# Performance work log

Measured on AMD Instinct MI355X. Metric: run time of the kernel, lower is better.

The kernel has to match this reference:

```python
import jax, jax.numpy as jnp
import numpy as np

N_LAYER = 4
N_HEAD = 8
D_HEAD = 64
D_MODEL = 512
D_INNER = 2048
NMT = 16  # num_mem_tokens
BSZ = 1
QLEN = 2048


def _rel_shift(x):
    # x: [i, j, b, n] -> Transformer-XL relative shift
    i, j, b, n = x.shape
    zero_pad = jnp.zeros((i, 1, b, n), dtype=x.dtype)
    x_padded = jnp.concatenate([zero_pad, x], axis=1)  # [i, j+1, b, n]
    x_padded = x_padded.reshape(j + 1, i, b, n)
    return x_padded[1:].reshape(i, j, b, n)


def _layer_norm(x, g, b):
    mu = jnp.mean(x, axis=-1, keepdims=True)
    var = jnp.mean(jnp.square(x - mu), axis=-1, keepdims=True)
    return (x - mu) / jnp.sqrt(var + 1e-5) * g + b


def setup_inputs() -> dict:
    key = jax.random.key(0)
    ks = jax.random.split(key, 12)
    s = 0.02
    return {
        "word_emb": jax.random.normal(ks[0], (BSZ, QLEN, D_MODEL), jnp.float32),
        "mem_tokens": jax.random.normal(ks[1], (NMT, BSZ, D_MODEL), jnp.float32),
        "Wqkv": jax.random.normal(ks[2], (N_LAYER, D_MODEL, 3 * N_HEAD * D_HEAD), jnp.float32) * s,
        "Wr": jax.random.normal(ks[3], (N_LAYER, D_MODEL, N_HEAD * D_HEAD), jnp.float32) * s,
        "Wo": jax.random.normal(ks[4], (N_LAYER, N_HEAD * D_HEAD, D_MODEL), jnp.float32) * s,
        "ln1_scale": jnp.ones((N_LAYER, D_MODEL), jnp.float32),
        "ln1_bias": jnp.zeros((N_LAYER, D_MODEL), jnp.float32),
        "ffn_W1": jax.random.normal(ks[5], (N_LAYER, D_MODEL, D_INNER), jnp.float32) * s,
        "ffn_b1": jnp.zeros((N_LAYER, D_INNER), jnp.float32),
        "ffn_W2": jax.random.normal(ks[6], (N_LAYER, D_INNER, D_MODEL), jnp.float32) * s,
        "ffn_b2": jnp.zeros((N_LAYER, D_MODEL), jnp.float32),
        "ln2_scale": jnp.ones((N_LAYER, D_MODEL), jnp.float32),
        "ln2_bias": jnp.zeros((N_LAYER, D_MODEL), jnp.float32),
        "r_w_bias": jax.random.normal(ks[7], (N_HEAD, D_HEAD), jnp.float32) * s,
        "r_r_bias": jax.random.normal(ks[8], (N_HEAD, D_HEAD), jnp.float32) * s,
    }


def reference(word_emb, mem_tokens, Wqkv, Wr, Wo, ln1_scale, ln1_bias,
              ffn_W1, ffn_b1, ffn_W2, ffn_b2, ln2_scale, ln2_bias,
              r_w_bias, r_r_bias):
    # word_emb: [B, Q, D] -> [Q, B, D]; prepend + append mem tokens (mem_at_end)
    w = jnp.transpose(word_emb, (1, 0, 2))
    w = jnp.concatenate([mem_tokens, w, mem_tokens], axis=0)  # [T, B, D]
    T, B = w.shape[0], w.shape[1]

    # causal mask (mlen=0) with mem-token exceptions, True = masked
    mask = jnp.triu(jnp.ones((T, T), dtype=bool), k=1)
    mask = mask.at[:NMT, :NMT].set(False)          # read-mem block attends to itself
    mask = mask.at[-NMT:, -NMT:].set(False)        # write-mem block attends to itself

    # sinusoidal relative positional embedding, pos_seq = T-1 .. 0
    inv_freq = 1.0 / (10000.0 ** (jnp.arange(0, D_MODEL, 2, dtype=jnp.float32) / D_MODEL))
    pos_seq = jnp.arange(T - 1, -1, -1.0, dtype=jnp.float32)
    sinusoid = pos_seq[:, None] * inv_freq[None, :]
    pos_emb = jnp.concatenate([jnp.sin(sinusoid), jnp.cos(sinusoid)], axis=-1)  # [T, D]

    scale = 1.0 / np.sqrt(D_HEAD)
    for l in range(N_LAYER):
        heads = w @ Wqkv[l]                                        # [T, B, 3*H*Dh]
        q, k, v = jnp.split(heads, 3, axis=-1)
        q = q.reshape(T, B, N_HEAD, D_HEAD)
        k = k.reshape(T, B, N_HEAD, D_HEAD)
        v = v.reshape(T, B, N_HEAD, D_HEAD)
        r = (pos_emb @ Wr[l]).reshape(T, N_HEAD, D_HEAD)           # [T, H, Dh]

        AC = jnp.einsum('ibnd,jbnd->ijbn', q + r_w_bias, k)
        BD = _rel_shift(jnp.einsum('ibnd,jnd->ijbn', q + r_r_bias, r))
        score = (AC + BD) * scale                                  # [T, T, B, H]
        score = jnp.where(mask[:, :, None, None], -1e30, score)
        prob = jax.nn.softmax(score, axis=1)
        attn_vec = jnp.einsum('ijbn,jbnd->ibnd', prob, v).reshape(T, B, N_HEAD * D_HEAD)

        w = _layer_norm(w + attn_vec @ Wo[l], ln1_scale[l], ln1_bias[l])  # post-LN
        ff = jax.nn.relu(w @ ffn_W1[l] + ffn_b1[l]) @ ffn_W2[l] + ffn_b2[l]
        w = _layer_norm(w + ff, ln2_scale[l], ln2_bias[l])
    return w  # [T, B, D]
```

## Files before the change

### kernel.cpp

```cpp
#include <hip/hip_runtime.h>
#include <hip/hip_bf16.h>
#include <math.h>

#define TT 2080
#define DM 512
#define DI 2048
#define NH 8
#define DH 64
#define NMTOK 16
#define NLAYER 4
#define QKV_N 1536
#define ATT_SCALE 0.125f
#define SPLIT 8
#define WT_STRIDE 3407872
#define QRP_HEAD 2200640

typedef short bf16x8 __attribute__((ext_vector_type(8)));
typedef float f32x4 __attribute__((ext_vector_type(4)));
typedef unsigned short ushort_t;

__device__ __forceinline__ ushort_t f2bf(float f) {
  __hip_bfloat16 h = __float2bfloat16(f);
  return *reinterpret_cast<ushort_t*>(&h);
}
__device__ __forceinline__ float bfbits2f(unsigned int hi_bits) {
  return __uint_as_float(hi_bits);
}
__device__ __forceinline__ float bf2f(ushort_t u) {
  return bfbits2f(((unsigned int)u) << 16);
}
__device__ __forceinline__ void unpack8(uint4 v, float* f) {
  f[0] = bfbits2f(v.x << 16); f[1] = bfbits2f(v.x & 0xffff0000u);
  f[2] = bfbits2f(v.y << 16); f[3] = bfbits2f(v.y & 0xffff0000u);
  f[4] = bfbits2f(v.z << 16); f[5] = bfbits2f(v.z & 0xffff0000u);
  f[6] = bfbits2f(v.w << 16); f[7] = bfbits2f(v.w & 0xffff0000u);
}
__device__ __forceinline__ unsigned int pack2(ushort_t lo, ushort_t hi) {
  return (unsigned int)lo | ((unsigned int)hi << 16);
}
__device__ __forceinline__ void barrier_lds() {
  asm volatile("s_waitcnt lgkmcnt(0)" ::: "memory");
  __builtin_amdgcn_s_barrier();
}
__device__ __forceinline__ size_t qr_rowbase(int i) {
  int m = i & 3;
  int r = (m == 0) ? 0 : (m == 1) ? 3 : (m == 2) ? 5 : 6;
  return (size_t)i * (i + 33) / 2 + 6 * (i >> 2) + r;
}

__global__ __launch_bounds__(256) void k_prep(
    const float* __restrict__ Wqkv, const float* __restrict__ Wr,
    const float* __restrict__ Wo, const float* __restrict__ W1,
    const float* __restrict__ W2, ushort_t* __restrict__ dstAll,
    const float* __restrict__ we, const float* __restrict__ mem,
    float* __restrict__ w, ushort_t* __restrict__ wb,
    ushort_t* __restrict__ posb) {
  const int tid = threadIdx.x;
  if (blockIdx.x >= 13312) {
    int idx = (blockIdx.x - 13312) * 256 + tid;
    if (idx >= TT * DM) return;
    int t = idx >> 9, d = idx & 511;
    float v;
    if (t < NMTOK) v = mem[t * DM + d];
    else if (t < NMTOK + 2048) v = we[(t - NMTOK) * DM + d];
    else v = mem[(t - (NMTOK + 2048)) * DM + d];
    w[idx] = v;
    wb[idx] = f2bf(v);
    float p = (float)(TT - 1 - t);
    int i2 = d & 255;
    float freq = 1.0f / powf(10000.f, ((float)(2 * i2)) / 512.f);
    float ang = p * freq;
    posb[idx] = f2bf((d < 256) ? sinf(ang) : cosf(ang));
    return;
  }
  __shared__ float tl[32][33];
  const int l = blockIdx.x / 3328;
  int idx = blockIdx.x % 3328;
  const float* src;
  ushort_t* dst = dstAll + (size_t)l * WT_STRIDE;
  int K, N, local;
  if (idx < 768)       { src = Wqkv + (size_t)l * 512 * 1536; K = 512;  N = 1536; local = idx; }
  else if (idx < 1024) { src = Wr   + (size_t)l * 512 * 512;  dst += 786432;  K = 512;  N = 512;  local = idx - 768; }
  else if (idx < 1280) { src = Wo   + (size_t)l * 512 * 512;  dst += 1048576; K = 512;  N = 512;  local = idx - 1024; }
  else if (idx < 2304) { src = W1   + (size_t)l * 512 * 2048; dst += 1310720; K = 512;  N = 2048; local = idx - 1280; }
  else                 { src = W2   + (size_t)l * 2048 * 512; dst += 2359296; K = 2048; N = 512;  local = idx - 2304; }
  const int ntiles = N / 32;
  const int n0 = (local % ntiles) * 32, k0 = (local / ntiles) * 32;
#pragma unroll
  for (int p = 0; p < 4; ++p) {
    int row = (tid >> 5) + 8 * p, col = tid & 31;
    tl[row][col] = src[(size_t)(k0 + row) * N + n0 + col];
  }
  __syncthreads();
#pragma unroll
  for (int p = 0; p < 4; ++p) {
    int n = (tid >> 5) + 8 * p, k = tid & 31;
    dst[(size_t)(n0 + n) * K + k0 + k] = f2bf(tl[k][n]);
  }
}

__device__ __forceinline__ void gemm32x64_body(const ushort_t* __restrict__ A,
                                               const ushort_t* __restrict__ Bt,
                                               const float* __restrict__ bias,
                                               float* __restrict__ C,
                                               ushort_t* __restrict__ Cb,
                                               ushort_t* __restrict__ qrb,
                                               const float* __restrict__ rrb,
                                               int N, int K, int flags,
                                               int m0, int n0) {
  __shared__ short As[32][72];
  __shared__ short Bs[64][72];
  const int tid = threadIdx.x;
  const int lane = tid & 63, wv = tid >> 6;
  const int wm = (wv >> 1) * 16, wn = (wv & 1) * 32;
  const int lm = lane & 15, quad = lane >> 4;
  const int sr = tid >> 3, sc8 = (tid & 7) * 8;

  f32x4 acc[2];
  acc[0] = (f32x4)(0.f); acc[1] = (f32x4)(0.f);

  auto loadA = [&](int k0) -> uint4 {
    return *(const uint4*)&A[(size_t)(m0 + sr) * K + k0 + sc8];
  };
  auto loadB = [&](int row, int k0) -> uint4 {
    return *(const uint4*)&Bt[(size_t)(n0 + row) * K + k0 + sc8];
  };

  uint4 aC = loadA(0), b0C = loadB(sr, 0), b1C = loadB(sr + 32, 0);

  for (int k0 = 0; k0 < K; k0 += 64) {
    const int kn = (k0 + 64 < K) ? k0 + 64 : k0;
    uint4 aN = loadA(kn), b0N = loadB(sr, kn), b1N = loadB(sr + 32, kn);
    barrier_lds();
    *(uint4*)&As[sr][sc8] = aC;
    *(uint4*)&Bs[sr][sc8] = b0C;
    *(uint4*)&Bs[sr + 32][sc8] = b1C;
    barrier_lds();
#pragma unroll
    for (int kk = 0; kk < 64; kk += 32) {
      bf16x8 a = *(const bf16x8*)&As[wm + lm][kk + quad * 8];
      bf16x8 b0 = *(const bf16x8*)&Bs[wn + lm][kk + quad * 8];
      bf16x8 b1 = *(const bf16x8*)&Bs[wn + 16 + lm][kk + quad * 8];
      acc[0] = __builtin_amdgcn_mfma_f32_16x16x32_bf16(a, b0, acc[0], 0, 0, 0);
      acc[1] = __builtin_amdgcn_mfma_f32_16x16x32_bf16(a, b1, acc[1], 0, 0, 0);
    }
    aC = aN; b0C = b0N; b1C = b1N;
  }
#pragma unroll
  for (int nt = 0; nt < 2; ++nt) {
    int col = n0 + wn + nt * 16 + lm;
    float bv = (flags & 1) ? bias[col] : 0.f;
#pragma unroll
    for (int t = 0; t < 4; ++t) {
      int row = m0 + wm + quad * 4 + t;
      float v = acc[nt][t] + bv;
      if (flags & 2) v = fmaxf(v, 0.f);
      if (flags & 4) Cb[(size_t)row * N + col] = f2bf(v);
      else C[(size_t)row * N + col] = v;
      if ((flags & 8) && col < DM)
        qrb[(size_t)row * DM + col] = f2bf(v + rrb[col]);
    }
  }
}

__global__ __launch_bounds__(256) void k_gemm_mfma(const ushort_t* __restrict__ A,
                                                   const ushort_t* __restrict__ Bt,
                                                   const float* __restrict__ bias,
                                                   float* __restrict__ C,
                                                   ushort_t* __restrict__ Cb,
                                                   int N, int K, int flags) {
  gemm32x64_body(A, Bt, bias, C, Cb, nullptr, nullptr, N, K, flags,
                 blockIdx.y * 32, blockIdx.x * 64);
}

__global__ __launch_bounds__(256) void k_gemm_qkvwr(const ushort_t* __restrict__ wb,
                                                    const ushort_t* __restrict__ posb,
                                                    const ushort_t* __restrict__ qkvT,
                                                    const ushort_t* __restrict__ wrT,
                                                    ushort_t* __restrict__ qkvb,
                                                    ushort_t* __restrict__ rbg,
                                                    ushort_t* __restrict__ qrb,
                                                    const float* __restrict__ rrb) {
  const int bx = blockIdx.x;
  if (bx < 24)
    gemm32x64_body(wb, qkvT, nullptr, nullptr, qkvb, qrb, rrb, QKV_N, DM,
                   (bx < 8) ? (4 | 8) : 4, blockIdx.y * 32, bx * 64);
  else
    gemm32x64_body(posb, wrT, nullptr, nullptr, rbg, nullptr, nullptr, DM, DM, 4,
                   blockIdx.y * 32, (bx - 24) * 64);
}

__global__ __launch_bounds__(256) void k_qr(const ushort_t* __restrict__ qrb,
                                            const ushort_t* __restrict__ rbg,
                                            ushort_t* __restrict__ qrp) {
  const int h = blockIdx.z;
  const int m0 = blockIdx.y * 32, n0 = blockIdx.x * 64;
  if (!(n0 == 0 || n0 + 63 >= TT - 32 - m0)) return;
  __shared__ short As[32][72];
  __shared__ short Bs[64][72];
  const int tid = threadIdx.x;
  const int lane = tid & 63, wv = tid >> 6;
  const int wm = (wv >> 1) * 16, wn = (wv & 1) * 32;
  const int lm = lane & 15, quad = lane >> 4;
  const int sr = tid >> 3, sc8 = (tid & 7) * 8;
  const uint4 zero4 = make_uint4(0, 0, 0, 0);

  *(uint4*)&As[sr][sc8] = *(const uint4*)&qrb[(size_t)(m0 + sr) * DM + h * DH + sc8];
  int br0 = n0 + sr, br1 = n0 + sr + 32;
  *(uint4*)&Bs[sr][sc8] =
      (br0 < TT) ? *(const uint4*)&rbg[(size_t)br0 * DM + h * DH + sc8] : zero4;
  *(uint4*)&Bs[sr + 32][sc8] =
      (br1 < TT) ? *(const uint4*)&rbg[(size_t)br1 * DM + h * DH + sc8] : zero4;
  __syncthreads();

  f32x4 acc[2];
  acc[0] = (f32x4)(0.f); acc[1] = (f32x4)(0.f);
#pragma unroll
  for (int kk = 0; kk < 64; kk += 32) {
    bf16x8 a = *(const bf16x8*)&As[wm + lm][kk + quad * 8];
    bf16x8 b0 = *(const bf16x8*)&Bs[wn + lm][kk + quad * 8];
    bf16x8 b1 = *(const bf16x8*)&Bs[wn + 16 + lm][kk + quad * 8];
    acc[0] = __builtin_amdgcn_mfma_f32_16x16x32_bf16(a, b0, acc[0], 0, 0, 0);
    acc[1] = __builtin_amdgcn_mfma_f32_16x16x32_bf16(a, b1, acc[1], 0, 0, 0);
  }
  const size_t hb = (size_t)h * QRP_HEAD;
#pragma unroll
  for (int nt = 0; nt < 2; ++nt) {
    int col = n0 + wn + nt * 16 + lm;
    if (col >= TT) continue;
#pragma unroll
    for (int t = 0; t < 4; ++t) {
      int row = m0 + wm + quad * 4 + t;
      float v = acc[nt][t];
      int p = row + col - (TT - 1);
      size_t rb = hb + qr_rowbase(row);
      if (p >= 0) qrp[rb + p] = f2bf(v);
      if (col < 16) qrp[rb + row + 1 + col] = f2bf(v);
    }
  }
}

__global__ __launch_bounds__(256) void k_attn(const ushort_t* __restrict__ qkv,
                                              const ushort_t* __restrict__ qrp,
                                              const float* __restrict__ rwb,
                                              float* __restrict__ mlP,
                                              ushort_t* __restrict__ opP) {
  const int h = blockIdx.y;
  const int qt = 64 - blockIdx.x;
  const int c = blockIdx.z;
  if (c > qt) return;
  const int i0 = qt * 32;
  const int tid = threadIdx.x;
  const int lane = tid & 63, wv = tid >> 6;
  const int lm = lane & 15, quad = lane >> 4;

  __shared__ short qw[32][72];
  __shared__ short ks_[32][72];
  __shared__ short vsT[64][70];
  __shared__ short pb[32][40];
  __shared__ float st[32][33];
  __shared__ float m_s[32], l_s[32], alpha_s[32];

  const int krr = tid >> 3, kc8 = (tid & 7) * 8;
  const int vrr = tid >> 4, vc4 = tid & 15;
  const int ii = tid >> 3, g = tid & 7, jjb = g * 4;
  const int i = i0 + ii;
  const size_t hb = (size_t)h * QRP_HEAD;
  const size_t qrRow = hb + qr_rowbase(i);
  const size_t qrRowW = hb + qr_rowbase(i + 1) + i + 2;

  auto loadK = [&](int j0) -> uint4 {
    return *(const uint4*)&qkv[(size_t)(j0 + krr) * QKV_N + DM + h * DH + kc8];
  };

  {
    uint4 qv = *(const uint4*)&qkv[(size_t)(i0 + krr) * QKV_N + h * DH + kc8];
    float f[8]; unpack8(qv, f);
    float4 w0 = *(const float4*)&rwb[h * DH + kc8];
    float4 w1 = *(const float4*)&rwb[h * DH + kc8 + 4];
    uint4 ow;
    ow.x = pack2(f2bf(f[0] + w0.x), f2bf(f[1] + w0.y));
    ow.y = pack2(f2bf(f[2] + w0.z), f2bf(f[3] + w0.w));
    ow.z = pack2(f2bf(f[4] + w1.x), f2bf(f[5] + w1.y));
    ow.w = pack2(f2bf(f[6] + w1.z), f2bf(f[7] + w1.w));
    *(uint4*)&qw[krr][kc8] = ow;
  }
  if (tid < 32) { m_s[tid] = -INFINITY; l_s[tid] = 0.f; }

  f32x4 oA = (f32x4)(0.f);
  f32x4 oB = (f32x4)(0.f);

  uint4 kcur = loadK(c * 32);
  const ushort_t* vp0 = &qkv[(size_t)(c * 32 + 2 * vrr) * QKV_N + 2 * DM + h * DH + vc4 * 4];
  uint2 v0cur = *(const uint2*)vp0, v1cur = *(const uint2*)(vp0 + QKV_N);

  for (int jt = c; jt <= qt; jt += SPLIT) {
    const int j0 = jt * 32;
    uint2 qr2 = *(const uint2*)&qrp[qrRow + j0 + jjb];
    const int jn = (jt + SPLIT <= qt) ? jt + SPLIT : jt;
    uint4 knext = loadK(jn * 32);
    const ushort_t* vpn = &qkv[(size_t)(jn * 32 + 2 * vrr) * QKV_N + 2 * DM + h * DH + vc4 * 4];
    uint2 v0n = *(const uint2*)vpn, v1n = *(const uint2*)(vpn + QKV_N);

    barrier_lds();
    *(uint4*)&ks_[krr][kc8] = kcur;
    {
      ushort_t a0 = (ushort_t)(v0cur.x & 0xffffu), a1 = (ushort_t)(v0cur.x >> 16);
      ushort_t a2 = (ushort_t)(v0cur.y & 0xffffu), a3 = (ushort_t)(v0cur.y >> 16);
      ushort_t c0 = (ushort_t)(v1cur.x & 0xffffu), c1 = (ushort_t)(v1cur.x >> 16);
      ushort_t c2 = (ushort_t)(v1cur.y & 0xffffu), c3 = (ushort_t)(v1cur.y >> 16);
      *(unsigned int*)&vsT[vc4 * 4 + 0][2 * vrr] = pack2(a0, c0);
      *(unsigned int*)&vsT[vc4 * 4 + 1][2 * vrr] = pack2(a1, c1);
      *(unsigned int*)&vsT[vc4 * 4 + 2][2 * vrr] = pack2(a2, c2);
      *(unsigned int*)&vsT[vc4 * 4 + 3][2 * vrr] = pack2(a3, c3);
    }
    barrier_lds();

    {
      const int acit = wv >> 1, acjt = wv & 1;
      f32x4 ac = (f32x4)(0.f);
#pragma unroll
      for (int k2 = 0; k2 < 64; k2 += 32) {
        bf16x8 a = *(const bf16x8*)&qw[acit * 16 + lm][k2 + quad * 8];
        bf16x8 b = *(const bf16x8*)&ks_[acjt * 16 + lm][k2 + quad * 8];
        ac = __builtin_amdgcn_mfma_f32_16x16x32_bf16(a, b, ac, 0, 0, 0);
      }
#pragma unroll
      for (int t = 0; t < 4; ++t)
        st[acit * 16 + quad * 4 + t][acjt * 16 + lm] = ac[t];
    }
    barrier_lds();

    {
      float bd4[4];
      bd4[0] = bf2f((ushort_t)(qr2.x & 0xffffu));
      bd4[1] = bf2f((ushort_t)(qr2.x >> 16));
      bd4[2] = bf2f((ushort_t)(qr2.y & 0xffffu));
      bd4[3] = bf2f((ushort_t)(qr2.y >> 16));
      float sreg[4];
#pragma unroll
      for (int u = 0; u < 4; ++u) {
        int j = j0 + jjb + u;
        float acv = st[ii][jjb + u];
        float s;
        if (j <= i) {
          s = (acv + bd4[u]) * ATT_SCALE;
        } else {
          bool inmem = (i < NMTOK && j < NMTOK) ||
                       (i >= TT - NMTOK && j >= TT - NMTOK);
          if (!inmem) s = -1e30f;
          else if (j == i + 1) s = acv * ATT_SCALE;
          else s = (acv + bf2f(qrp[qrRowW + (j - i - 2)])) * ATT_SCALE;
        }
        sreg[u] = s;
      }
      float tmax = fmaxf(fmaxf(sreg[0], sreg[1]), fmaxf(sreg[2], sreg[3]));
#pragma unroll
      for (int off = 1; off < 8; off <<= 1) tmax = fmaxf(tmax, __shfl_xor(tmax, off));
      const float mold = m_s[ii];
      const float mnew = fmaxf(mold, tmax);
      const float alpha = __expf(mold - mnew);
      float p[4], psum = 0.f;
#pragma unroll
      for (int u = 0; u < 4; ++u) { p[u] = __expf(sreg[u] - mnew); psum += p[u]; }
#pragma unroll
      for (int off = 1; off < 8; off <<= 1) psum += __shfl_xor(psum, off);
      uint2 pk;
      pk.x = pack2(f2bf(p[0]), f2bf(p[1]));
      pk.y = pack2(f2bf(p[2]), f2bf(p[3]));
      *(uint2*)&pb[ii][jjb] = pk;
      if (g == 0) {
        m_s[ii] = mnew;
        l_s[ii] = l_s[ii] * alpha + psum;
        alpha_s[ii] = alpha;
      }
    }
    barrier_lds();

    {
      float a0 = alpha_s[lm], a1 = alpha_s[16 + lm];
      union { bf16x8 v; unsigned int u[4]; } av;
      const unsigned int* vp = (const unsigned int*)&vsT[wv * 16 + lm][quad * 8];
      av.u[0] = vp[0]; av.u[1] = vp[1]; av.u[2] = vp[2]; av.u[3] = vp[3];
      bf16x8 p0 = *(const bf16x8*)&pb[lm][quad * 8];
      bf16x8 p1 = *(const bf16x8*)&pb[16 + lm][quad * 8];
#pragma unroll
      for (int t = 0; t < 4; ++t) { oA[t] *= a0; oB[t] *= a1; }
      oA = __builtin_amdgcn_mfma_f32_16x16x32_bf16(av.v, p0, oA, 0, 0, 0);
      oB = __builtin_amdgcn_mfma_f32_16x16x32_bf16(av.v, p1, oB, 0, 0, 0);
    }
    kcur = knext; v0cur = v0n; v1cur = v1n;
  }

  {
    const int pidx = (qt * NH + h) * SPLIT + c;
    if (tid < 32) {
      mlP[(size_t)pidx * 64 + tid] = m_s[tid];
      mlP[(size_t)pidx * 64 + 32 + tid] = l_s[tid];
    }
    ushort_t o0[4], o1[4];
#pragma unroll
    for (int t = 0; t < 4; ++t) { o0[t] = f2bf(oA[t]); o1[t] = f2bf(oB[t]); }
    size_t ob = (size_t)pidx * 2048;
    *(uint2*)&opP[ob + (size_t)lm * 64 + wv * 16 + quad * 4] = *(uint2*)o0;
    *(uint2*)&opP[ob + (size_t)(16 + lm) * 64 + wv * 16 + quad * 4] = *(uint2*)o1;
  }
}

__global__ __launch_bounds__(256) void k_attn_combine(const float* __restrict__ mlP,
                                                      const ushort_t* __restrict__ opP,
                                                      ushort_t* __restrict__ attnb) {
  const int qt = blockIdx.x, h = blockIdx.y;
  const int nc = (qt + 1 < SPLIT) ? qt + 1 : SPLIT;
  const int tid = threadIdx.x;
  const int i = tid >> 3, d8 = (tid & 7) * 8;
  const size_t base = (size_t)(qt * NH + h) * SPLIT;
  float m[SPLIT], l[SPLIT], wgt[SPLIT];
  float M = -INFINITY;
  for (int cc = 0; cc < nc; ++cc) {
    m[cc] = mlP[(base + cc) * 64 + i];
    l[cc] = mlP[(base + cc) * 64 + 32 + i];
    M = fmaxf(M, m[cc]);
  }
  float L = 0.f;
  for (int cc = 0; cc < nc; ++cc) { wgt[cc] = __expf(m[cc] - M); L += l[cc] * wgt[cc]; }
  float acc[8] = {0, 0, 0, 0, 0, 0, 0, 0};
  for (int cc = 0; cc < nc; ++cc) {
    uint4 v = *(const uint4*)&opP[(base + cc) * 2048 + (size_t)i * 64 + d8];
    float f[8]; unpack8(v, f);
#pragma unroll
    for (int k = 0; k < 8; ++k) acc[k] += wgt[cc] * f[k];
  }
  const float inv = 1.f / L;
  ushort_t o8[8];
#pragma unroll
  for (int k = 0; k < 8; ++k) o8[k] = f2bf(acc[k] * inv);
  *(uint4*)&attnb[(size_t)(qt * 32 + i) * DM + h * DH + d8] = *(uint4*)o8;
}

__global__ __launch_bounds__(256) void k_addln(const float* __restrict__ w,
                                               float* __restrict__ wout,
                                               ushort_t* __restrict__ wb,
                                               const float* __restrict__ delta,
                                               const float* __restrict__ gamma,
                                               const float* __restrict__ beta) {
  const int row = blockIdx.x;
  const int tid = threadIdx.x;
  __shared__ float red[4], red2[4];
  size_t base = (size_t)row * DM;
  float x0 = w[base + tid] + delta[base + tid];
  float x1 = w[base + tid + 256] + delta[base + tid + 256];
  float s = x0 + x1;
#pragma unroll
  for (int off = 1; off < 64; off <<= 1) s += __shfl_xor(s, off);
  if ((tid & 63) == 0) red[tid >> 6] = s;
  __syncthreads();
  float mu = (red[0] + red[1] + red[2] + red[3]) * (1.f / 512.f);
  float d0 = x0 - mu, d1 = x1 - mu;
  float v = d0 * d0 + d1 * d1;
#pragma unroll
  for (int off = 1; off < 64; off <<= 1) v += __shfl_xor(v, off);
  if ((tid & 63) == 0) red2[tid >> 6] = v;
  __syncthreads();
  float var = (red2[0] + red2[1] + red2[2] + red2[3]) * (1.f / 512.f);
  float rstd = rsqrtf(var + 1e-5f);
  float o0 = d0 * rstd * gamma[tid] + beta[tid];
  float o1 = d1 * rstd * gamma[tid + 256] + beta[tid + 256];
  wout[base + tid] = o0;
  wout[base + tid + 256] = o1;
  wb[base + tid] = f2bf(o0);
  wb[base + tid + 256] = f2bf(o1);
}

extern "C" void kernel_launch(void* const* d_in, const int* in_sizes, int n_in,
                              void* d_out, int out_size, void* d_ws, size_t ws_size,
                              hipStream_t stream) {
  const float* we   = (const float*)d_in[0];
  const float* mem  = (const float*)d_in[1];
  const float* Wqkv = (const float*)d_in[2];
  const float* Wr   = (const float*)d_in[3];
  const float* Wo   = (const float*)d_in[4];
  const float* ln1s = (const float*)d_in[5];
  const float* ln1b = (const float*)d_in[6];
  const float* W1   = (const float*)d_in[7];
  const float* b1   = (const float*)d_in[8];
  const float* W2   = (const float*)d_in[9];
  const float* b2   = (const float*)d_in[10];
  const float* ln2s = (const float*)d_in[11];
  const float* ln2b = (const float*)d_in[12];
  const float* rwb  = (const float*)d_in[13];
  const float* rrb  = (const float*)d_in[14];

  float* w     = (float*)d_ws;
  float* proj  = w + (size_t)TT * DM;
  ushort_t* wb    = (ushort_t*)(proj + (size_t)TT * DM);
  ushort_t* posb  = wb + (size_t)TT * DM;
  ushort_t* attnb = posb + (size_t)TT * DM;
  ushort_t* qkvb  = attnb + (size_t)TT * DM;
  ushort_t* rbg   = qkvb + (size_t)TT * QKV_N;
  ushort_t* WtAll = rbg + (size_t)TT * DM;
  ushort_t* opP   = WtAll + (size_t)NLAYER * WT_STRIDE;
  float* mlP   = (float*)(opP + (size_t)65 * 8 * SPLIT * 2048);
  ushort_t* qrb  = (ushort_t*)(mlP + (size_t)65 * 8 * SPLIT * 64);
  ushort_t* qrp  = qrb + (size_t)TT * DM;
  ushort_t* ff1b  = qkvb;
  float* ff2   = proj;
  const size_t OFF_QKVT = 0, OFF_WRT = 786432, OFF_WOT = 1048576,
               OFF_W1T = 1310720, OFF_W2T = 2359296;

  k_prep<<<13312 + 4160, 256, 0, stream>>>(Wqkv, Wr, Wo, W1, W2, WtAll,
                                           we, mem, w, wb, posb);

  dim3 gQW(32, 65);
  dim3 gDM32(DM / 64, 65);
  dim3 gDI32(DI / 64, 65);
  dim3 gQR(33, 65, NH);
  dim3 gA(65, NH, SPLIT);
  dim3 gC(65, NH);

  for (int l = 0; l < NLAYER; ++l) {
    const ushort_t* Wt = WtAll + (size_t)l * WT_STRIDE;
    k_gemm_qkvwr<<<gQW, 256, 0, stream>>>(wb, posb, Wt + OFF_QKVT,
                                          Wt + OFF_WRT, qkvb, rbg, qrb, rrb);
    k_qr<<<gQR, 256, 0, stream>>>(qrb, rbg, qrp);
    k_attn<<<gA, 256, 0, stream>>>(qkvb, qrp, rwb, mlP, opP);
    k_attn_combine<<<gC, 256, 0, stream>>>(mlP, opP, attnb);
    k_gemm_mfma<<<gDM32, 256, 0, stream>>>(attnb, Wt + OFF_WOT, nullptr, proj, nullptr,
                                           DM, DM, 0);
    k_addln<<<TT, 256, 0, stream>>>(w, w, wb, proj,
                                    ln1s + (size_t)l * DM, ln1b + (size_t)l * DM);
    k_gemm_mfma<<<gDI32, 256, 0, stream>>>(wb, Wt + OFF_W1T, b1 + (size_t)l * DI, nullptr, ff1b,
                                           DI, DM, 1 | 2 | 4);
    k_gemm_mfma<<<gDM32, 256, 0, stream>>>(ff1b, Wt + OFF_W2T, b2 + (size_t)l * DM, ff2, nullptr,
                                           DM, DI, 1);
    float* wout = (l == NLAYER - 1) ? (float*)d_out : w;
    k_addln<<<TT, 256, 0, stream>>>(w, wout, wb, ff2,
                                    ln2s + (size_t)l * DM, ln2b + (size_t)l * DM);
  }
}
```

Measured before the change: 634.1 us.

## Use MFMA-fragment-tiled layout and 128x128 LDS-DMA GEMMs for QKV and FFN

Activations, positional embeddings and most transposed weights are now stored in a fragment-tiled layout (16 rows by 32 k-values per 512-element block). This lets new 128x128 GEMM kernels copy tiles straight into LDS with global_load_lds and feed MFMA without reshuffling. The QKV/Wr projection and FFN1 replace the old 32x64 tile kernel. FFN2 uses a 4-way split-K whose partial sums are reduced inside the following add+LayerNorm kernel. The aim is more data reuse per tile and less load overhead, at the cost of clamped overlapping edge tiles and extra partial-sum traffic.

```diff
diff --git a/kernel.cpp b/kernel.cpp
--- a/kernel.cpp
+++ b/kernel.cpp
@@ -1,6 +1,7 @@
 #include <hip/hip_runtime.h>
 #include <hip/hip_bf16.h>
 #include <math.h>
+#include <stdint.h>
 
 #define TT 2080
 #define DM 512
@@ -42,10 +43,19 @@
   asm volatile("s_waitcnt lgkmcnt(0)" ::: "memory");
   __builtin_amdgcn_s_barrier();
 }
+__device__ __forceinline__ void gload16(const ushort_t* g, ushort_t* l) {
+  __builtin_amdgcn_global_load_lds(
+      (__attribute__((address_space(1))) void*)(uintptr_t)g,
+      (__attribute__((address_space(3))) void*)(uintptr_t)l, 16, 0, 0);
+}
 __device__ __forceinline__ size_t qr_rowbase(int i) {
   int m = i & 3;
   int r = (m == 0) ? 0 : (m == 1) ? 3 : (m == 2) ? 5 : 6;
   return (size_t)i * (i + 33) / 2 + 6 * (i >> 2) + r;
+}
+__device__ __forceinline__ size_t ft512(int r, int c) {
+  return (((size_t)(r >> 4) * 16 + (c >> 5)) << 9) + (((c >> 3) & 3) << 7) +
+         ((r & 15) << 3) + (c & 7);
 }
 
 __global__ __launch_bounds__(256) void k_prep(
@@ -53,8 +63,8 @@
     const float* __restrict__ Wo, const float* __restrict__ W1,
     const float* __restrict__ W2, ushort_t* __restrict__ dstAll,
     const float* __restrict__ we, const float* __restrict__ mem,
-    float* __restrict__ w, ushort_t* __restrict__ wb,
-    ushort_t* __restrict__ posb) {
+    float* __restrict__ w, ushort_t* __restrict__ wbft,
+    ushort_t* __restrict__ posft) {
   const int tid = threadIdx.x;
   if (blockIdx.x >= 13312) {
     int idx = (blockIdx.x - 13312) * 256 + tid;
@@ -65,12 +75,12 @@
     else if (t < NMTOK + 2048) v = we[(t - NMTOK) * DM + d];
     else v = mem[(t - (NMTOK + 2048)) * DM + d];
     w[idx] = v;
-    wb[idx] = f2bf(v);
+    wbft[ft512(t, d)] = f2bf(v);
     float p = (float)(TT - 1 - t);
     int i2 = d & 255;
     float freq = 1.0f / powf(10000.f, ((float)(2 * i2)) / 512.f);
     float ang = p * freq;
-    posb[idx] = f2bf((d < 256) ? sinf(ang) : cosf(ang));
+    posft[ft512(t, d)] = f2bf((d < 256) ? sinf(ang) : cosf(ang));
     return;
   }
   __shared__ float tl[32][33];
@@ -79,9 +89,10 @@
   const float* src;
   ushort_t* dst = dstAll + (size_t)l * WT_STRIDE;
   int K, N, local;
+  bool isFT = true;
   if (idx < 768)       { src = Wqkv + (size_t)l * 512 * 1536; K = 512;  N = 1536; local = idx; }
   else if (idx < 1024) { src = Wr   + (size_t)l * 512 * 512;  dst += 786432;  K = 512;  N = 512;  local = idx - 768; }
-  else if (idx < 1280) { src = Wo   + (size_t)l * 512 * 512;  dst += 1048576; K = 512;  N = 512;  local = idx - 1024; }
+  else if (idx < 1280) { src = Wo   + (size_t)l * 512 * 512;  dst += 1048576; K = 512;  N = 512;  local = idx - 1024; isFT = false; }
   else if (idx < 2304) { src = W1   + (size_t)l * 512 * 2048; dst += 1310720; K = 512;  N = 2048; local = idx - 1280; }
   else                 { src = W2   + (size_t)l * 2048 * 512; dst += 2359296; K = 2048; N = 512;  local = idx - 2304; }
   const int ntiles = N / 32;
@@ -92,10 +103,24 @@
     tl[row][col] = src[(size_t)(k0 + row) * N + n0 + col];
   }
   __syncthreads();
-#pragma unroll
-  for (int p = 0; p < 4; ++p) {
-    int n = (tid >> 5) + 8 * p, k = tid & 31;
-    dst[(size_t)(n0 + n) * K + k0 + k] = f2bf(tl[k][n]);
+  if (isFT) {
+    if (tid < 128) {
+      int b = tid >> 6, l2 = tid & 63;
+      int nn = b * 16 + (l2 & 15);
+      int kq = (l2 >> 4) * 8;
+      ushort_t t8[8];
+#pragma unroll
+      for (int e = 0; e < 8; ++e) t8[e] = f2bf(tl[kq + e][nn]);
+      size_t ad = (((size_t)((n0 >> 4) + b) * (K >> 5) + (k0 >> 5)) << 9) +
+                  ((size_t)l2 << 3);
+      *(uint4*)&dst[ad] = *(uint4*)t8;
+    }
+  } else {
+#pragma unroll
+    for (int p = 0; p < 4; ++p) {
+      int n = (tid >> 5) + 8 * p, k = tid & 31;
+      dst[(size_t)(n0 + n) * K + k0 + k] = f2bf(tl[k][n]);
+    }
   }
 }
 
@@ -104,8 +129,6 @@
                                                const float* __restrict__ bias,
                                                float* __restrict__ C,
                                                ushort_t* __restrict__ Cb,
-                                               ushort_t* __restrict__ qrb,
-                                               const float* __restrict__ rrb,
                                                int N, int K, int flags,
                                                int m0, int n0) {
   __shared__ short As[32][72];
@@ -157,8 +180,6 @@
       if (flags & 2) v = fmaxf(v, 0.f);
       if (flags & 4) Cb[(size_t)row * N + col] = f2bf(v);
       else C[(size_t)row * N + col] = v;
-      if ((flags & 8) && col < DM)
-        qrb[(size_t)row * DM + col] = f2bf(v + rrb[col]);
     }
   }
 }
@@ -169,25 +190,138 @@
                                                    float* __restrict__ C,
                                                    ushort_t* __restrict__ Cb,
                                                    int N, int K, int flags) {
-  gemm32x64_body(A, Bt, bias, C, Cb, nullptr, nullptr, N, K, flags,
-                 blockIdx.y * 32, blockIdx.x * 64);
-}
-
-__global__ __launch_bounds__(256) void k_gemm_qkvwr(const ushort_t* __restrict__ wb,
-                                                    const ushort_t* __restrict__ posb,
-                                                    const ushort_t* __restrict__ qkvT,
-                                                    const ushort_t* __restrict__ wrT,
-                                                    ushort_t* __restrict__ qkvb,
-                                                    ushort_t* __restrict__ rbg,
-                                                    ushort_t* __restrict__ qrb,
-                                                    const float* __restrict__ rrb) {
+  gemm32x64_body(A, Bt, bias, C, Cb, N, K, flags, blockIdx.y * 32, blockIdx.x * 64);
+}
+
+__device__ __forceinline__ void gemm_ft_body(
+    ushort_t* smem, const ushort_t* __restrict__ A, const ushort_t* __restrict__ Bt,
+    const float* __restrict__ bias, int N, int K, int kBeg, int kEnd,
+    int m0, int n0, int flags,
+    float* __restrict__ Cf, ushort_t* __restrict__ Crm,
+    ushort_t* __restrict__ Cft, int cftKT,
+    ushort_t* __restrict__ qrb, const float* __restrict__ rrb) {
+  const int tid = threadIdx.x;
+  const int lane = tid & 63, wv = tid >> 6;
+  const int wm = (wv >> 1) * 64, wn = (wv & 1) * 64;
+  const int lm = lane & 15, quad = lane >> 4;
+  const int AKT = K >> 5;
+  const int mt0 = m0 >> 4, nt0 = n0 >> 4;
+  const int kt0 = kBeg >> 5;
+
+  f32x4 acc[4][4];
+#pragma unroll
+  for (int i = 0; i < 4; ++i)
+#pragma unroll
+    for (int j = 0; j < 4; ++j) acc[i][j] = (f32x4)(0.f);
+
+  auto stage = [&](ushort_t* dA, int ktg) {
+    ushort_t* dB = dA + 8192;
+#pragma unroll
+    for (int it = 0; it < 4; ++it) {
+      const int c = (it << 8) + tid;
+      const int blk = c >> 6, ln = c & 63;
+      gload16(A + (((size_t)(mt0 + (blk >> 1)) * AKT + ktg + (blk & 1)) << 9) + (ln << 3),
+              dA + (c << 3));
+      gload16(Bt + (((size_t)(nt0 + (blk >> 1)) * AKT + ktg + (blk & 1)) << 9) + (ln << 3),
+              dB + (c << 3));
+    }
+  };
+  auto compute = [&](const ushort_t* dA) {
+    const ushort_t* dB = dA + 8192;
+#pragma unroll
+    for (int kk = 0; kk < 2; ++kk) {
+      bf16x8 a[4], b[4];
+#pragma unroll
+      for (int i = 0; i < 4; ++i)
+        a[i] = *(const bf16x8*)&dA[((((wm >> 4) + i) << 1) + kk) * 512 + (lane << 3)];
+#pragma unroll
+      for (int j = 0; j < 4; ++j)
+        b[j] = *(const bf16x8*)&dB[((((wn >> 4) + j) << 1) + kk) * 512 + (lane << 3)];
+#pragma unroll
+      for (int i = 0; i < 4; ++i)
+#pragma unroll
+        for (int j = 0; j < 4; ++j)
+          acc[i][j] = __builtin_amdgcn_mfma_f32_16x16x32_bf16(a[i], b[j], acc[i][j], 0, 0, 0);
+    }
+  };
+
+  const int nIter = (kEnd - kBeg) >> 6;
+  stage(smem, kt0);
+  __syncthreads();
+  for (int t = 0; t < nIter; t += 2) {
+    if (t + 1 < nIter) stage(smem + 16384, kt0 + (t + 1) * 2);
+    compute(smem);
+    __syncthreads();
+    if (t + 2 < nIter) stage(smem, kt0 + (t + 2) * 2);
+    compute(smem + 16384);
+    __syncthreads();
+  }
+
+#pragma unroll
+  for (int i = 0; i < 4; ++i) {
+    const int rowb = m0 + wm + i * 16 + quad * 4;
+#pragma unroll
+    for (int j = 0; j < 4; ++j) {
+      const int col = n0 + wn + j * 16 + lm;
+      const float bv = (flags & 1) ? bias[col] : 0.f;
+#pragma unroll
+      for (int t2 = 0; t2 < 4; ++t2) {
+        const int row = rowb + t2;
+        float v = acc[i][j][t2] + bv;
+        if (flags & 2) v = fmaxf(v, 0.f);
+        if (Cft) {
+          Cft[(((size_t)(row >> 4) * cftKT + (col >> 5)) << 9) +
+              (((col >> 3) & 3) << 7) + ((row & 15) << 3) + (col & 7)] = f2bf(v);
+        } else if (Crm) {
+          Crm[(size_t)row * N + col] = f2bf(v);
+        } else {
+          Cf[(size_t)row * N + col] = v;
+        }
+        if (flags & 8) qrb[(size_t)row * DM + col] = f2bf(v + rrb[col]);
+      }
+    }
+  }
+}
+
+__global__ __launch_bounds__(256) void k_gemm_qkvwr_ft(
+    const ushort_t* __restrict__ wbft, const ushort_t* __restrict__ posft,
+    const ushort_t* __restrict__ qkvT, const ushort_t* __restrict__ wrT,
+    ushort_t* __restrict__ qkvb, ushort_t* __restrict__ rbg,
+    ushort_t* __restrict__ qrb, const float* __restrict__ rrb) {
+  __shared__ ushort_t smem[32768];
+  int m0 = blockIdx.y * 128;
+  if (m0 + 128 > TT) m0 = TT - 128;
   const int bx = blockIdx.x;
-  if (bx < 24)
-    gemm32x64_body(wb, qkvT, nullptr, nullptr, qkvb, qrb, rrb, QKV_N, DM,
-                   (bx < 8) ? (4 | 8) : 4, blockIdx.y * 32, bx * 64);
+  if (bx < 12)
+    gemm_ft_body(smem, wbft, qkvT, nullptr, QKV_N, DM, 0, DM, m0, bx * 128,
+                 (bx < 4) ? 8 : 0, nullptr, qkvb, nullptr, 0, qrb, rrb);
   else
-    gemm32x64_body(posb, wrT, nullptr, nullptr, rbg, nullptr, nullptr, DM, DM, 4,
-                   blockIdx.y * 32, (bx - 24) * 64);
+    gemm_ft_body(smem, posft, wrT, nullptr, DM, DM, 0, DM, m0, (bx - 12) * 128,
+                 0, nullptr, rbg, nullptr, 0, nullptr, nullptr);
+}
+
+__global__ __launch_bounds__(256) void k_ffn1_ft(const ushort_t* __restrict__ wbft,
+                                                 const ushort_t* __restrict__ w1T,
+                                                 const float* __restrict__ b1l,
+                                                 ushort_t* __restrict__ ff1ft) {
+  __shared__ ushort_t smem[32768];
+  int m0 = blockIdx.y * 128;
+  if (m0 + 128 > TT) m0 = TT - 128;
+  gemm_ft_body(smem, wbft, w1T, b1l, DI, DM, 0, DM, m0, blockIdx.x * 128,
+               1 | 2, nullptr, nullptr, ff1ft, DI >> 5, nullptr, nullptr);
+}
+
+__global__ __launch_bounds__(256) void k_ffn2_ft(const ushort_t* __restrict__ ff1ft,
+                                                 const ushort_t* __restrict__ w2T,
+                                                 const float* __restrict__ b2l,
+                                                 float* __restrict__ ff2p) {
+  __shared__ ushort_t smem[32768];
+  int m0 = blockIdx.y * 128;
+  if (m0 + 128 > TT) m0 = TT - 128;
+  const int s = blockIdx.z;
+  gemm_ft_body(smem, ff1ft, w2T, b2l, DM, DI, s * 512, s * 512 + 512, m0,
+               blockIdx.x * 128, (s == 0) ? 1 : 0,
+               ff2p + (size_t)s * TT * DM, nullptr, nullptr, 0, nullptr, nullptr);
 }
 
 __global__ __launch_bounds__(256) void k_qr(const ushort_t* __restrict__ qrb,
@@ -440,16 +574,22 @@
 
 __global__ __launch_bounds__(256) void k_addln(const float* __restrict__ w,
                                                float* __restrict__ wout,
-                                               ushort_t* __restrict__ wb,
+                                               ushort_t* __restrict__ wbft,
                                                const float* __restrict__ delta,
+                                               int nparts,
                                                const float* __restrict__ gamma,
                                                const float* __restrict__ beta) {
   const int row = blockIdx.x;
   const int tid = threadIdx.x;
   __shared__ float red[4], red2[4];
+  __shared__ float sm[512];
   size_t base = (size_t)row * DM;
-  float x0 = w[base + tid] + delta[base + tid];
-  float x1 = w[base + tid + 256] + delta[base + tid + 256];
+  float x0 = w[base + tid];
+  float x1 = w[base + tid + 256];
+  for (int p = 0; p < nparts; ++p) {
+    x0 += delta[(size_t)p * TT * DM + base + tid];
+    x1 += delta[(size_t)p * TT * DM + base + tid + 256];
+  }
   float s = x0 + x1;
 #pragma unroll
   for (int off = 1; off < 64; off <<= 1) s += __shfl_xor(s, off);
@@ -468,8 +608,15 @@
   float o1 = d1 * rstd * gamma[tid + 256] + beta[tid + 256];
   wout[base + tid] = o0;
   wout[base + tid + 256] = o1;
-  wb[base + tid] = f2bf(o0);
-  wb[base + tid + 256] = f2bf(o1);
+  sm[tid] = o0; sm[tid + 256] = o1;
+  __syncthreads();
+  if (tid < 64) {
+    const int d8 = tid << 3;
+    ushort_t t8[8];
+#pragma unroll
+    for (int e = 0; e < 8; ++e) t8[e] = f2bf(sm[d8 + e]);
+    *(uint4*)&wbft[ft512(row, d8)] = *(uint4*)t8;
+  }
 }
 
 extern "C" void kernel_launch(void* const* d_in, const int* in_sizes, int n_in,
@@ -493,9 +640,9 @@
 
   float* w     = (float*)d_ws;
   float* proj  = w + (size_t)TT * DM;
-  ushort_t* wb    = (ushort_t*)(proj + (size_t)TT * DM);
-  ushort_t* posb  = wb + (size_t)TT * DM;
-  ushort_t* attnb = posb + (size_t)TT * DM;
+  ushort_t* wbft  = (ushort_t*)(proj + (size_t)TT * DM);
+  ushort_t* posft = wbft + (size_t)TT * DM;
+  ushort_t* attnb = posft + (size_t)TT * DM;
   ushort_t* qkvb  = attnb + (size_t)TT * DM;
   ushort_t* rbg   = qkvb + (size_t)TT * QKV_N;
   ushort_t* WtAll = rbg + (size_t)TT * DM;
@@ -503,38 +650,37 @@
   float* mlP   = (float*)(opP + (size_t)65 * 8 * SPLIT * 2048);
   ushort_t* qrb  = (ushort_t*)(mlP + (size_t)65 * 8 * SPLIT * 64);
   ushort_t* qrp  = qrb + (size_t)TT * DM;
-  ushort_t* ff1b  = qkvb;
-  float* ff2   = proj;
+  ushort_t* ff1ft = qkvb;
+  float* ff2p  = (float*)opP;
   const size_t OFF_QKVT = 0, OFF_WRT = 786432, OFF_WOT = 1048576,
                OFF_W1T = 1310720, OFF_W2T = 2359296;
 
   k_prep<<<13312 + 4160, 256, 0, stream>>>(Wqkv, Wr, Wo, W1, W2, WtAll,
-                                           we, mem, w, wb, posb);
-
-  dim3 gQW(32, 65);
+                                           we, mem, w, wbft, posft);
+
+  dim3 gQW(16, 17);
+  dim3 gW1(16, 17);
+  dim3 gW2(4, 17, 4);
   dim3 gDM32(DM / 64, 65);
-  dim3 gDI32(DI / 64, 65);
   dim3 gQR(33, 65, NH);
   dim3 gA(65, NH, SPLIT);
   dim3 gC(65, NH);
 
   for (int l = 0; l < NLAYER; ++l) {
     const ushort_t* Wt = WtAll + (size_t)l * WT_STRIDE;
-    k_gemm_qkvwr<<<gQW, 256, 0, stream>>>(wb, posb, Wt + OFF_QKVT,
-                                          Wt + OFF_WRT, qkvb, rbg, qrb, rrb);
+    k_gemm_qkvwr_ft<<<gQW, 256, 0, stream>>>(wbft, posft, Wt + OFF_QKVT,
+                                             Wt + OFF_WRT, qkvb, rbg, qrb, rrb);
     k_qr<<<gQR, 256, 0, stream>>>(qrb, rbg, qrp);
     k_attn<<<gA, 256, 0, stream>>>(qkvb, qrp, rwb, mlP, opP);
     k_attn_combine<<<gC, 256, 0, stream>>>(mlP, opP, attnb);
     k_gemm_mfma<<<gDM32, 256, 0, stream>>>(attnb, Wt + OFF_WOT, nullptr, proj, nullptr,
                                            DM, DM, 0);
-    k_addln<<<TT, 256, 0, stream>>>(w, w, wb, proj,
+    k_addln<<<TT, 256, 0, stream>>>(w, w, wbft, proj, 1,
                                     ln1s + (size_t)l * DM, ln1b + (size_t)l * DM);
-    k_gemm_mfma<<<gDI32, 256, 0, stream>>>(wb, Wt + OFF_W1T, b1 + (size_t)l * DI, nullptr, ff1b,
-                                           DI, DM, 1 | 2 | 4);
-    k_gemm_mfma<<<gDM32, 256, 0, stream>>>(ff1b, Wt + OFF_W2T, b2 + (size_t)l * DM, ff2, nullptr,
-                                           DM, DI, 1);
+    k_ffn1_ft<<<gW1, 256, 0, stream>>>(wbft, Wt + OFF_W1T, b1 + (size_t)l * DI, ff1ft);
+    k_ffn2_ft<<<gW2, 256, 0, stream>>>(ff1ft, Wt + OFF_W2T, b2 + (size_t)l * DM, ff2p);
     float* wout = (l == NLAYER - 1) ? (float*)d_out : w;
-    k_addln<<<TT, 256, 0, stream>>>(w, wout, wb, ff2,
+    k_addln<<<TT, 256, 0, stream>>>(w, wout, wbft, ff2p, 4,
                                     ln2s + (size_t)l * DM, ln2b + (size_t)l * DM);
   }
 }
```

New measurement: 662.9 us. +4.5%, slower.
